# Kernel optimization log

Measured on AMD Instinct MI355X. Metric: run time of the kernel, lower is better.

The kernel has to match this reference:

```python
import jax, jax.numpy as jnp
import numpy as np

N_P, N_D, N_S = 100000, 1000, 5000      # patients, drugs, diseases
C, H, L = 64, 4, 2                       # hidden, heads, layers
DH = C // H                              # head dim
IN_P, IN_D, IN_S = 64, 128, 64           # raw feature dims per node type
E_PD, E_DP, E_DS, E_PS = 300000, 300000, 100000, 100000
EPS = 1e-16


def setup_inputs() -> dict:
    key = jax.random.key(0)
    ks = jax.random.split(key, 20)

    def lin(k, fin, fout, prefix=()):
        return jax.random.normal(k, prefix + (fin, fout), jnp.float32) / np.sqrt(fin).astype(np.float32)

    def edges(k, e, n_src, n_dst):
        k1, k2 = jax.random.split(k)
        return jnp.stack([jax.random.randint(k1, (e,), 0, n_src),
                          jax.random.randint(k2, (e,), 0, n_dst)]).astype(jnp.int32)

    inp = {}
    inp['x_p'] = jax.random.normal(ks[0], (N_P, IN_P), jnp.float32)
    inp['x_d'] = jax.random.normal(ks[1], (N_D, IN_D), jnp.float32)
    inp['x_s'] = jax.random.normal(ks[2], (N_S, IN_S), jnp.float32)
    inp['Win_p'] = lin(ks[3], IN_P, C); inp['bin_p'] = jnp.zeros((C,), jnp.float32)
    inp['Win_d'] = lin(ks[4], IN_D, C); inp['bin_d'] = jnp.zeros((C,), jnp.float32)
    inp['Win_s'] = lin(ks[5], IN_S, C); inp['bin_s'] = jnp.zeros((C,), jnp.float32)
    inp['Wk'] = lin(ks[6], C, C, (L, 3)); inp['bk'] = jnp.zeros((L, 3, C), jnp.float32)
    inp['Wq'] = lin(ks[7], C, C, (L, 3)); inp['bq'] = jnp.zeros((L, 3, C), jnp.float32)
    inp['Wv'] = lin(ks[8], C, C, (L, 3)); inp['bv'] = jnp.zeros((L, 3, C), jnp.float32)
    inp['Wa'] = lin(ks[9], C, C, (L, 3)); inp['ba'] = jnp.zeros((L, 3, C), jnp.float32)
    inp['a_rel'] = jax.random.normal(ks[10], (L, 4, H, DH, DH), jnp.float32) / np.sqrt(DH).astype(np.float32)
    inp['m_rel'] = jax.random.normal(ks[11], (L, 4, H, DH, DH), jnp.float32) / np.sqrt(DH).astype(np.float32)
    inp['p_rel'] = jnp.ones((L, 4, H), jnp.float32)   # PyG inits rel prior to ones
    inp['skip'] = jnp.ones((L, 3), jnp.float32)       # PyG inits skip gate to ones
    inp['ei_pd'] = edges(ks[12], E_PD, N_P, N_D)  # patient -takes-> drug
    inp['ei_dp'] = edges(ks[13], E_DP, N_D, N_P)  # drug -taken_by-> patient
    inp['ei_ds'] = edges(ks[14], E_DS, N_D, N_S)  # drug -treats-> disease
    inp['ei_ps'] = edges(ks[15], E_PS, N_P, N_S)  # patient -has-> disease
    return inp


def _hgt(x_p, x_d, x_s, Win_p, bin_p, Win_d, bin_d, Win_s, bin_s,
         Wk, bk, Wq, bq, Wv, bv, Wa, ba, a_rel, m_rel, p_rel, skip,
         ei_pd, ei_dp, ei_ds, ei_ps):
    Ns = (N_P, N_D, N_S)
    # per-node-type input projection (lin_dict)
    xs = [x_p @ Win_p + bin_p, x_d @ Win_d + bin_d, x_s @ Win_s + bin_s]
    # (src_type, dst_type, edge_index) for each relation
    edge_defs = [(0, 1, ei_pd), (1, 0, ei_dp), (1, 2, ei_ds), (0, 2, ei_ps)]
    inv_sqrt_d = np.float32(1.0 / np.sqrt(DH))

    for l in range(L):  # HGTConv layers
        k_t = [(xs[t] @ Wk[l, t] + bk[l, t]).reshape(Ns[t], H, DH) for t in range(3)]
        q_t = [(xs[t] @ Wq[l, t] + bq[l, t]).reshape(Ns[t], H, DH) for t in range(3)]
        v_t = [(xs[t] @ Wv[l, t] + bv[l, t]).reshape(Ns[t], H, DH) for t in range(3)]
        out = [jnp.zeros((Ns[t], H, DH), xs[t].dtype) for t in range(3)]
        for r, (st, dt, ei) in enumerate(edge_defs):
            src, dst = ei[0], ei[1]
            # relation-specific head-wise transforms of K and V
            k_rel = jnp.einsum('nhd,hde->nhe', k_t[st], a_rel[l, r])
            v_rel = jnp.einsum('nhd,hde->nhe', v_t[st], m_rel[l, r])
            # attention logits per edge, per head: [E, H]
            alpha = (q_t[dt][dst] * k_rel[src]).sum(-1) * (p_rel[l, r] * inv_sqrt_d)
            # segment softmax over incoming edges of each dst node (per relation)
            mx = jax.ops.segment_max(alpha, dst, num_segments=Ns[dt])
            a = jnp.exp(alpha - jax.lax.stop_gradient(mx)[dst])
            den = jax.ops.segment_sum(a, dst, num_segments=Ns[dt])
            a = a / (den[dst] + EPS)
            # attention-weighted scatter-add of messages, grouped by 'sum'
            out[dt] = out[dt] + jax.ops.segment_sum(v_rel[src] * a[:, :, None], dst, num_segments=Ns[dt])
        new_xs = []
        for t in range(3):
            o = jax.nn.gelu(out[t].reshape(Ns[t], C), approximate=False) @ Wa[l, t] + ba[l, t]
            s = jax.nn.sigmoid(skip[l, t])  # learned skip gate (in == out channels)
            new_xs.append(s * o + (1.0 - s) * xs[t])
        xs = new_xs
    # concatenate node-type outputs along node axis: [N_P+N_D+N_S, C]
    return jnp.concatenate(xs, axis=0)


def reference(x_p, x_d, x_s, Win_p, bin_p, Win_d, bin_d, Win_s, bin_s,
              Wk, bk, Wq, bq, Wv, bv, Wa, ba, a_rel, m_rel, p_rel, skip,
              ei_pd, ei_dp, ei_ds, ei_ps):
    return _hgt(x_p, x_d, x_s, Win_p, bin_p, Win_d, bin_d, Win_s, bin_s,
                Wk, bk, Wq, bq, Wv, bv, Wa, ba, a_rel, m_rel, p_rel, skip,
                ei_pd, ei_dp, ei_ds, ei_ps)
```

## Files before the change

kernel.cpp:

```cpp
#include <hip/hip_runtime.h>
#include <cmath>

typedef unsigned short ush;
typedef __attribute__((ext_vector_type(8))) short short8;
typedef __attribute__((ext_vector_type(4))) float floatx4;

static constexpr int N_P = 100000, N_D = 1000, N_S = 5000, NT = N_P + N_D + N_S;
static constexpr int NC = 111000;
static constexpr int E_TOT = 800000;

static constexpr int NB0 = 128, NB2 = 64, NB3 = 64;
static constexpr int CH0 = (300000 + NB0 - 1) / NB0;
static constexpr int CH2 = (100000 + NB2 - 1) / NB2;
static constexpr int HB0_OFF = 0;
static constexpr int HB2_OFF = NB0 * 1000;
static constexpr int HB3_OFF = HB2_OFF + NB2 * 5000;
static constexpr int NCH0 = NB0 / 16, NCH2 = NB2 / 16;
static constexpr int CS0_OFF = 0;
static constexpr int CS2_OFF = NCH0 * 1000;
static constexpr int CS3_OFF = CS2_OFF + NCH2 * 5000;
static constexpr int NHIST = NB0 + NB2 + NB3;
static constexpr int NBLK_R1 = (300000 + 255) / 256;
static constexpr int NZB = (100000 + 255) / 256;

__device__ __forceinline__ float b2f(ush b) { return __uint_as_float(((unsigned)b) << 16); }
__device__ __forceinline__ ush f2b(float f) {
    unsigned u = __float_as_uint(f);
    return (ush)((u + 0x7FFFu + ((u >> 16) & 1u)) >> 16);
}

static constexpr size_t OFF_WINP = 0;
static constexpr size_t OFF_BINP = 4096;
static constexpr size_t OFF_WIND = 4160;
static constexpr size_t OFF_BIND = 12352;
static constexpr size_t OFF_WINS = 12416;
static constexpr size_t OFF_BINS = 16512;
static constexpr size_t OFF_WK = 16576;
static constexpr size_t OFF_BK = 41152;
static constexpr size_t OFF_WQ = 41536;
static constexpr size_t OFF_BQ = 66112;
static constexpr size_t OFF_WV = 66496;
static constexpr size_t OFF_BV = 91072;
static constexpr size_t OFF_WA = 91456;
static constexpr size_t OFF_BA = 116032;
static constexpr size_t OFF_AREL = 116416;
static constexpr size_t OFF_MREL = 124608;
static constexpr size_t OFF_PREL = 132800;
static constexpr size_t OFF_SKIP = 132832;
static constexpr size_t CW_TOTAL = 132838;
static constexpr int NCONVB = (int)((CW_TOTAL + 255) / 256);
static constexpr int NSCB = (NC + 1 + 255) / 256;

struct ConvArgs {
    const void* src[18];
    long cum[19];
    int fl[18];
};

struct CsrB {
    const int* ei[3];
    const int* ei1;
};

__device__ __forceinline__ void hist_geom(int b, const CsrB& c, int& r, const int*& ei, int& E,
                                          int& ndst, int& e0, int& e1, int& hb) {
    if (b < NB0) {
        r = 0; ei = c.ei[0]; E = 300000; ndst = 1000;
        e0 = b * CH0; hb = HB0_OFF + b * 1000;
    } else if (b < NB0 + NB2) {
        r = 1; ei = c.ei[1]; E = 100000; ndst = 5000;
        e0 = (b - NB0) * CH2; hb = HB2_OFF + (b - NB0) * 5000;
    } else {
        r = 2; ei = c.ei[2]; E = 100000; ndst = 5000;
        e0 = (b - NB0 - NB2) * CH2; hb = HB3_OFF + (b - NB0 - NB2) * 5000;
    }
    e1 = min(E, e0 + ((r == 0) ? CH0 : CH2));
}

__device__ __forceinline__ bool cs_geom(int g, int& idx0, int& step) {
    if (g >= 48000) return false;
    if (g < 8000) {
        int c = g / 1000, d = g % 1000;
        idx0 = HB0_OFF + c * 16 * 1000 + d; step = 1000;
    } else if (g < 28000) {
        int gg = g - 8000, c = gg / 5000, d = gg % 5000;
        idx0 = HB2_OFF + c * 16 * 5000 + d; step = 5000;
    } else {
        int gg = g - 28000, c = gg / 5000, d = gg % 5000;
        idx0 = HB3_OFF + c * 16 * 5000 + d; step = 5000;
    }
    return true;
}

__global__ __launch_bounds__(256) void k1_kernel(ConvArgs a, ush* __restrict__ dst,
                                                 int* __restrict__ cnt_r1, CsrB c,
                                                 int* __restrict__ HB) {
    const int b = blockIdx.x;
    if (b < NCONVB) {
        long g = (long)b * 256 + threadIdx.x;
        if (g >= (long)CW_TOTAL) return;
        int t = 0;
        while (g >= a.cum[t + 1]) t++;
        long i = g - a.cum[t];
        float v = a.fl[t] ? ((const float*)a.src[t])[i] : b2f(((const ush*)a.src[t])[i]);
        dst[g] = f2b(v);
    } else if (b < NCONVB + NZB) {
        int g = (b - NCONVB) * 256 + threadIdx.x;
        if (g < 100000) cnt_r1[g] = 0;
    } else {
        __shared__ int h[5000];
        int r, E, ndst, e0, e1, hb;
        const int* ei;
        hist_geom(b - NCONVB - NZB, c, r, ei, E, ndst, e0, e1, hb);
        for (int d = threadIdx.x; d < ndst; d += 256) h[d] = 0;
        __syncthreads();
        for (int e = e0 + threadIdx.x; e < e1; e += 256) atomicAdd(&h[ei[E + e]], 1);
        __syncthreads();
        for (int d = threadIdx.x; d < ndst; d += 256) HB[hb + d] = h[d];
    }
}

template <int K>
__device__ __forceinline__ void stage_A(short* sA, const ush* __restrict__ X, int M, int row0) {
    for (int cid = threadIdx.x; cid < 64 * K / 8; cid += 256) {
        int r = cid / (K / 8), c0 = (cid % (K / 8)) * 8;
        int row = row0 + r;
        short8 v = {0, 0, 0, 0, 0, 0, 0, 0};
        if (row < M) v = *(const short8*)(const void*)(X + (size_t)row * K + c0);
        *(short8*)(&sA[r * (K + 8) + c0]) = v;
    }
}

template <int K>
__device__ __forceinline__ void stage_A_raw(short* sA, const void* __restrict__ X, int f,
                                            int M, int row0) {
    for (int cid = threadIdx.x; cid < 64 * K / 8; cid += 256) {
        int r = cid / (K / 8), c0 = (cid % (K / 8)) * 8;
        int row = row0 + r;
        short8 v = {0, 0, 0, 0, 0, 0, 0, 0};
        if (row < M) {
            if (f) {
                const floatx4* fp = (const floatx4*)((const float*)X + (size_t)row * K + c0);
                floatx4 f0 = fp[0], f1 = fp[1];
#pragma unroll
                for (int j = 0; j < 4; j++) v[j] = (short)f2b(f0[j]);
#pragma unroll
                for (int j = 0; j < 4; j++) v[4 + j] = (short)f2b(f1[j]);
            } else {
                v = *(const short8*)(const void*)((const ush*)X + (size_t)row * K + c0);
            }
        }
        *(short8*)(&sA[r * (K + 8) + c0]) = v;
    }
}

template <int K, int NOUT>
__device__ __forceinline__ void gemm_core(const short* sA, short* sB,
                                          const ush* __restrict__ W, const ush* __restrict__ Bb,
                                          ush* __restrict__ Y, int M, int row0) {
    constexpr int NF = (K / 32) * (NOUT / 16);
    const int tid = threadIdx.x;
    for (int u = tid; u < NF * 64; u += 256) {
        int f = u >> 6, l = u & 63;
        int s = f / (NOUT / 16), c = f % (NOUT / 16);
        int kbase = 32 * s + ((l >> 4) << 3), n = 16 * c + (l & 15);
        short8 v;
#pragma unroll
        for (int j = 0; j < 8; j++) v[j] = (short)W[(size_t)(kbase + j) * NOUT + n];
        *(short8*)(&sB[f * 512 + l * 8]) = v;
    }
    __syncthreads();
    const int w = tid >> 6, l = tid & 63;
    floatx4 acc[NOUT / 16];
#pragma unroll
    for (int c = 0; c < NOUT / 16; c++) {
        float bv = b2f(Bb[16 * c + (l & 15)]);
        acc[c] = (floatx4){bv, bv, bv, bv};
    }
#pragma unroll
    for (int s = 0; s < K / 32; s++) {
        short8 a = *(const short8*)(&sA[(16 * w + (l & 15)) * (K + 8) + 32 * s + ((l >> 4) << 3)]);
#pragma unroll
        for (int c = 0; c < NOUT / 16; c++) {
            short8 b = *(const short8*)(&sB[(s * (NOUT / 16) + c) * 512 + l * 8]);
            acc[c] = __builtin_amdgcn_mfma_f32_16x16x32_bf16(a, b, acc[c], 0, 0, 0);
        }
    }
#pragma unroll
    for (int c = 0; c < NOUT / 16; c++)
#pragma unroll
        for (int r = 0; r < 4; r++) {
            int row = row0 + 16 * w + ((l >> 4) << 2) + r;
            if (row < M) Y[(size_t)row * NOUT + 16 * c + (l & 15)] = f2b(acc[c][r]);
        }
}

template <int NG>
__device__ __forceinline__ void gemm_wide(const short* sA, short* sB,
                                          const ush* __restrict__ Wq, const ush* __restrict__ Bq,
                                          ush* __restrict__ Yq,
                                          const ush* __restrict__ WeA, ush* __restrict__ YA,
                                          const ush* __restrict__ WeB, ush* __restrict__ YB,
                                          int M, int row0) {
    constexpr int NF = 2 * NG;
    const int tid = threadIdx.x;
    for (int u = tid; u < NF * 64; u += 256) {
        int f = u >> 6, l = u & 63;
        int s = f / NG, c = f % NG;
        int kbase = 32 * s + ((l >> 4) << 3);
        const ush* W; int ld, cw;
        if (c < 4) { W = Wq; ld = 64; cw = 16 * c; }
        else if (c < 12) { W = WeA; ld = 128; cw = 16 * (c - 4); }
        else { W = WeB; ld = 128; cw = 16 * (c - 12); }
        int n = cw + (l & 15);
        short8 v;
#pragma unroll
        for (int j = 0; j < 8; j++) v[j] = (short)W[(size_t)(kbase + j) * ld + n];
        *(short8*)(&sB[f * 512 + l * 8]) = v;
    }
    __syncthreads();
    const int w = tid >> 6, l = tid & 63;
    floatx4 acc[NG];
#pragma unroll
    for (int c = 0; c < NG; c++) {
        float bv;
        if (c < 4) bv = b2f(Bq[16 * c + (l & 15)]);
        else if (c < 12) bv = b2f(WeA[8192 + 16 * (c - 4) + (l & 15)]);
        else bv = b2f(WeB[8192 + 16 * (c - 12) + (l & 15)]);
        acc[c] = (floatx4){bv, bv, bv, bv};
    }
#pragma unroll
    for (int s = 0; s < 2; s++) {
        short8 a = *(const short8*)(&sA[(16 * w + (l & 15)) * 72 + 32 * s + ((l >> 4) << 3)]);
#pragma unroll
        for (int c = 0; c < NG; c++) {
            short8 b = *(const short8*)(&sB[(s * NG + c) * 512 + l * 8]);
            acc[c] = __builtin_amdgcn_mfma_f32_16x16x32_bf16(a, b, acc[c], 0, 0, 0);
        }
    }
#pragma unroll
    for (int c = 0; c < NG; c++)
#pragma unroll
        for (int r = 0; r < 4; r++) {
            int row = row0 + 16 * w + ((l >> 4) << 2) + r;
            if (row >= M) continue;
            ush val = f2b(acc[c][r]);
            if (c < 4) Yq[(size_t)row * 64 + 16 * c + (l & 15)] = val;
            else if (c < 12) YA[(size_t)row * 128 + 16 * (c - 4) + (l & 15)] = val;
            else YB[(size_t)row * 128 + 16 * (c - 12) + (l & 15)] = val;
        }
}

struct K2Args {
    const void* raw[3];
    int f[3];
    const ush* W[3];
    const ush* Bb[3];
    ush* X;
    const int* HB;
    int* CS;
    int* cnt;
    const int* ei1;
};

__global__ __launch_bounds__(256) void k2_kernel(K2Args a) {
    extern __shared__ short smem[];
    const int b = blockIdx.x;
    if (b < 1658) {
        if (b < 1563) {
            short* sA = smem; short* sB = smem + 64 * 72;
            stage_A_raw<64>(sA, a.raw[0], a.f[0], N_P, b * 64);
            gemm_core<64, 64>(sA, sB, a.W[0], a.Bb[0], a.X, N_P, b * 64);
        } else if (b < 1579) {
            short* sA = smem; short* sB = smem + 64 * 136;
            stage_A_raw<128>(sA, a.raw[1], a.f[1], N_D, (b - 1563) * 64);
            gemm_core<128, 64>(sA, sB, a.W[1], a.Bb[1], a.X + (size_t)N_P * 64, N_D,
                               (b - 1563) * 64);
        } else {
            short* sA = smem; short* sB = smem + 64 * 72;
            stage_A_raw<64>(sA, a.raw[2], a.f[2], N_S, (b - 1579) * 64);
            gemm_core<64, 64>(sA, sB, a.W[2], a.Bb[2], a.X + (size_t)(N_P + N_D) * 64, N_S,
                              (b - 1579) * 64);
        }
    } else if (b < 1701) {
        int d = (b - 1658) * 256 + threadIdx.x;
        if (d >= 11000) return;
        int ld_, nch, base, step, cs0, csstep, roff;
        if (d < 1000) { ld_ = d; nch = NCH0; base = HB0_OFF + ld_; step = 1000;
                        cs0 = CS0_OFF + ld_; csstep = 1000; roff = 0; }
        else if (d < 6000) { ld_ = d - 1000; nch = NCH2; base = HB2_OFF + ld_; step = 5000;
                             cs0 = CS2_OFF + ld_; csstep = 5000; roff = 101000; }
        else { ld_ = d - 6000; nch = NCH2; base = HB3_OFF + ld_; step = 5000;
               cs0 = CS3_OFF + ld_; csstep = 5000; roff = 106000; }
        int run = 0;
        for (int cc = 0; cc < nch; cc++) {
            int s = 0;
#pragma unroll
            for (int bb = 0; bb < 16; bb++) s += a.HB[base + (cc * 16 + bb) * step];
            a.CS[cs0 + cc * csstep] = run;
            run += s;
        }
        a.cnt[roff + ld_] = run;
    } else {
        int g = (b - 1701) * 256 + threadIdx.x;
        if (g < 300000) atomicAdd(&a.cnt[1000 + a.ei1[300000 + g]], 1);
    }
}

__global__ __launch_bounds__(256) void k3_kernel(const int* __restrict__ cnt,
                                                 int* __restrict__ tmp,
                                                 int* __restrict__ part,
                                                 const ush* __restrict__ CW,
                                                 ush* __restrict__ weff) {
    const int b = blockIdx.x;
    if (b < 109) {
        __shared__ int ls[256];
        const int t = threadIdx.x;
        const int base = b * 1024 + t * 4;
        int v[4];
#pragma unroll
        for (int j = 0; j < 4; j++) v[j] = (base + j < NC) ? cnt[base + j] : 0;
        int tsum = v[0] + v[1] + v[2] + v[3];
        ls[t] = tsum;
        __syncthreads();
        for (int off = 1; off < 256; off <<= 1) {
            int y = (t >= off) ? ls[t - off] : 0;
            __syncthreads();
            ls[t] += y;
            __syncthreads();
        }
        int run = ls[t] - tsum;
#pragma unroll
        for (int j = 0; j < 4; j++) {
            if (base + j < NC) tmp[base + j] = run;
            run += v[j];
        }
        if (t == 255) part[b] = ls[255];
    } else {
        const int eb = b - 109;
        const int l = eb >> 2, r = eb & 3;
        const int st_of[4] = {0, 1, 1, 0};
        const int st = st_of[r];
        ush* out = weff + (size_t)eb * 8320;
        for (int idx = threadIdx.x; idx < 8320; idx += 256) {
            int n, k;
            if (idx < 8192) { k = idx >> 7; n = idx & 127; }
            else { k = -1; n = idx - 8192; }
            int kv = n >= 64;
            int j = n & 63, h = j >> 4, e = j & 15;
            const ush* W = CW + (kv ? OFF_WV : OFF_WK) + (size_t)(l * 3 + st) * 4096;
            const ush* B = CW + (kv ? OFF_BV : OFF_BK) + (size_t)(l * 3 + st) * 64;
            const ush* R = CW + (kv ? OFF_MREL : OFF_AREL) + (size_t)(l * 4 + r) * 1024;
            float acc = 0.f;
            if (k >= 0) {
#pragma unroll
                for (int d = 0; d < 16; d++)
                    acc += b2f(W[k * 64 + h * 16 + d]) * b2f(R[h * 256 + d * 16 + e]);
            } else {
#pragma unroll
                for (int d = 0; d < 16; d++)
                    acc += b2f(B[h * 16 + d]) * b2f(R[h * 256 + d * 16 + e]);
            }
            out[idx] = f2b(acc);
        }
    }
}

__global__ __launch_bounds__(256) void k4_kernel(const int* __restrict__ tmp,
                                                 const int* __restrict__ part,
                                                 int* __restrict__ rowptr,
                                                 int* __restrict__ HB,
                                                 const int* __restrict__ CS,
                                                 int* __restrict__ fillpos) {
    const int b = blockIdx.x;
    if (b < NSCB) {
        __shared__ int ls[256];
        const int t = threadIdx.x;
        ls[t] = (t < 109) ? part[t] : 0;
        __syncthreads();
        for (int off = 1; off < 256; off <<= 1) {
            int y = (t >= off) ? ls[t - off] : 0;
            __syncthreads();
            ls[t] += y;
            __syncthreads();
        }
        int i = b * 256 + t;
        if (i <= NC)
            rowptr[i] = (i == NC) ? ls[255] : tmp[i] + ((i >> 10) ? ls[(i >> 10) - 1] : 0);
    } else if (b < NSCB + 188) {
        int g = (b - NSCB) * 256 + threadIdx.x;
        int idx0, step;
        if (!cs_geom(g, idx0, step)) return;
        int run = CS[g];
#pragma unroll
        for (int bb = 0; bb < 16; bb++) {
            int t2 = HB[idx0 + bb * step];
            HB[idx0 + bb * step] = run;
            run += t2;
        }
    } else {
        int g = (b - NSCB - 188) * 256 + threadIdx.x;
        if (g < 100000) fillpos[g] = 0;
    }
}

struct QKVArgs {
    const ush* X;
    ush* Q;
    ush* KV[4];
    const ush* Wq[3];
    const ush* Bq[3];
    const ush* We[4];
    CsrB cb;
    const int* HB;
    const int* rowptr;
    int* fillpos;
    int* col;
};

__global__ __launch_bounds__(256) void qkvfill_kernel(QKVArgs a) {
    extern __shared__ short smem[];
    const int b = blockIdx.x;
    if (b < 1658) {
        short* sA = smem;
        short* sB = smem + 64 * 72;
        if (b < 1563) {
            stage_A<64>(sA, a.X, N_P, b * 64);
            gemm_wide<20>(sA, sB, a.Wq[0], a.Bq[0], a.Q, a.We[0], a.KV[0], a.We[3], a.KV[3],
                          N_P, b * 64);
        } else if (b < 1579) {
            int lb = b - 1563;
            stage_A<64>(sA, a.X + (size_t)N_P * 64, N_D, lb * 64);
            gemm_wide<20>(sA, sB, a.Wq[1], a.Bq[1], a.Q + (size_t)N_P * 64, a.We[1], a.KV[1],
                          a.We[2], a.KV[2], N_D, lb * 64);
        } else {
            int lb = b - 1579;
            stage_A<64>(sA, a.X + (size_t)(N_P + N_D) * 64, N_S, lb * 64);
            gemm_wide<4>(sA, sB, a.Wq[2], a.Bq[2], a.Q + (size_t)(N_P + N_D) * 64,
                         nullptr, nullptr, nullptr, nullptr, N_S, lb * 64);
        }
    } else if (b < 1658 + NHIST) {
        int* h = (int*)smem;
        int r, E, ndst, e0, e1, hb;
        const int* ei;
        hist_geom(b - 1658, a.cb, r, ei, E, ndst, e0, e1, hb);
        const int roff = (r == 0) ? 0 : (r == 1) ? 101000 : 106000;
        for (int d = threadIdx.x; d < ndst; d += 256) h[d] = a.rowptr[roff + d] + a.HB[hb + d];
        __syncthreads();
        for (int e = e0 + threadIdx.x; e < e1; e += 256) {
            int d = ei[E + e];
            int slot = atomicAdd(&h[d], 1);
            a.col[slot] = ei[e];
        }
    } else {
        int g = (b - 1658 - NHIST) * 256 + threadIdx.x;
        if (g < 300000) {
            int gi = 1000 + a.cb.ei1[300000 + g];
            int slot = a.rowptr[gi] + atomicAdd(&a.fillpos[gi], 1);
            a.col[slot] = a.cb.ei1[g];
        }
    }
}

struct AggrArgs {
    const int* rowptr;
    const int* col;
    const ush* KV[4];
    const ush* Q;
    const ush* prel;
    ush* OUT;
};

template <int LANES>
__device__ __forceinline__ void seg_attn(const AggrArgs& a, int rel, int g, int h, int lane,
                                         const float* qf, float* o) {
    const int s0 = a.rowptr[g], s1 = a.rowptr[g + 1];
    const ush* KV = a.KV[rel];
    const float ps = b2f(a.prel[rel * 4 + h]) * 0.25f;
    float m = -1e30f, s = 0.f;
    float acc[16];
#pragma unroll
    for (int i = 0; i < 16; i++) acc[i] = 0.f;
    for (int j = s0 + lane; j < s1; j += LANES) {
        int src = a.col[j];
        const ush* kp = KV + (size_t)src * 128 + h * 16;
        short8 k0 = *(const short8*)(const void*)kp;
        short8 k1 = *(const short8*)(const void*)(kp + 8);
        short8 v0 = *(const short8*)(const void*)(kp + 64);
        short8 v1 = *(const short8*)(const void*)(kp + 72);
        float dot = 0.f;
#pragma unroll
        for (int i = 0; i < 8; i++) dot += qf[i] * b2f((ush)k0[i]);
#pragma unroll
        for (int i = 0; i < 8; i++) dot += qf[8 + i] * b2f((ush)k1[i]);
        float aa = dot * ps;
        float nm = fmaxf(m, aa);
        float e0 = __expf(m - nm), e1 = __expf(aa - nm);
        s = s * e0 + e1;
#pragma unroll
        for (int i = 0; i < 8; i++) acc[i] = acc[i] * e0 + e1 * b2f((ush)v0[i]);
#pragma unroll
        for (int i = 0; i < 8; i++) acc[8 + i] = acc[8 + i] * e0 + e1 * b2f((ush)v1[i]);
        m = nm;
    }
#pragma unroll
    for (int wd = LANES >> 1; wd >= 1; wd >>= 1) {
        float mo = __shfl_xor(m, wd);
        float so = __shfl_xor(s, wd);
        float nm = fmaxf(m, mo);
        float e0 = __expf(m - nm), e1 = __expf(mo - nm);
        s = s * e0 + so * e1;
#pragma unroll
        for (int i = 0; i < 16; i++) {
            float ao = __shfl_xor(acc[i], wd);
            acc[i] = acc[i] * e0 + ao * e1;
        }
        m = nm;
    }
    float inv = 1.f / (s + 1e-16f);
#pragma unroll
    for (int i = 0; i < 16; i++) o[i] += acc[i] * inv;
}

template <int LANES>
__device__ __forceinline__ void job_run(const AggrArgs& a, int wid, int nd, int rel, int roff,
                                        size_t xoff, int rel2, int roff2) {
    const int lane = wid % LANES;
    const int grp = wid / LANES;
    const int d = grp >> 2, h = grp & 3;
    if (d >= nd) return;
    const ush* qp = a.Q + xoff + (size_t)d * 64 + h * 16;
    short8 q0 = *(const short8*)(const void*)qp;
    short8 q1 = *(const short8*)(const void*)(qp + 8);
    float qf[16];
#pragma unroll
    for (int i = 0; i < 8; i++) { qf[i] = b2f((ush)q0[i]); qf[8 + i] = b2f((ush)q1[i]); }
    float o[16];
#pragma unroll
    for (int i = 0; i < 16; i++) o[i] = 0.f;
    seg_attn<LANES>(a, rel, roff + d, h, lane, qf, o);
    if (rel2 >= 0) seg_attn<LANES>(a, rel2, roff2 + d, h, lane, qf, o);
    if (lane == 0) {
        ush* op = a.OUT + xoff + (size_t)d * 64 + h * 16;
        short8 w0, w1;
#pragma unroll
        for (int i = 0; i < 8; i++) {
            float va = o[i];
            w0[i] = (short)f2b(0.5f * va * (1.0f + erff(va * 0.70710678118654752f)));
            float vb = o[8 + i];
            w1[i] = (short)f2b(0.5f * vb * (1.0f + erff(vb * 0.70710678118654752f)));
        }
        *(short8*)(op) = w0;
        *(short8*)(op + 8) = w1;
    }
}

__global__ __launch_bounds__(256) void aggr_kernel(AggrArgs a) {
    const int b = blockIdx.x, t = threadIdx.x;
    if (b < 250) {
        job_run<16>(a, b * 256 + t, N_D, 0, 0, (size_t)N_P * 64, -1, 0);
    } else if (b < 563) {
        job_run<4>(a, (b - 250) * 256 + t, N_S, 2, 101000, (size_t)(N_P + N_D) * 64, 3, 106000);
    } else {
        job_run<2>(a, (b - 563) * 256 + t, N_P, 1, 1000, 0, -1, 0);
    }
}

struct EpiArgs {
    const ush* O;
    ush* X;
    const ush* W[3];
    const ush* Bb[3];
    const ush* skipv;
    void* fout;
    int foutf;
    int last;
};

__global__ __launch_bounds__(256) void epi_kernel(EpiArgs a) {
    const int b = blockIdx.x;
    int t, lb, M;
    size_t noff;
    if (b < 1563) { t = 0; lb = b; M = N_P; noff = 0; }
    else if (b < 1579) { t = 1; lb = b - 1563; M = N_D; noff = (size_t)N_P; }
    else { t = 2; lb = b - 1579; M = N_S; noff = (size_t)(N_P + N_D); }
    const ush* O = a.O + noff * 64;
    ush* X = a.X + noff * 64;
    const ush* W = a.W[t];
    __shared__ short sA[64 * 72];
    __shared__ short sB[8 * 512];
    const int tid = threadIdx.x;
    const int row0 = lb * 64;
    for (int cid = tid; cid < 512; cid += 256) {
        int r = cid >> 3, c0 = (cid & 7) * 8;
        int row = row0 + r;
        short8 sv = {0, 0, 0, 0, 0, 0, 0, 0};
        if (row < M) sv = *(const short8*)(const void*)(O + (size_t)row * 64 + c0);
        *(short8*)(&sA[r * 72 + c0]) = sv;
    }
    __syncthreads();
    const float sg = 1.f / (1.f + expf(-b2f(a.skipv[t])));
    for (int u = tid; u < 512; u += 256) {
        int f = u >> 6, l = u & 63;
        int s = f >> 2, c = f & 3;
        int kbase = 32 * s + ((l >> 4) << 3), n = 16 * c + (l & 15);
        short8 v;
#pragma unroll
        for (int j = 0; j < 8; j++) v[j] = (short)W[(size_t)(kbase + j) * 64 + n];
        *(short8*)(&sB[f * 512 + l * 8]) = v;
    }
    __syncthreads();
    const int w = tid >> 6, l = tid & 63;
    floatx4 acc[4];
#pragma unroll
    for (int c = 0; c < 4; c++) {
        float bv = b2f(a.Bb[t][16 * c + (l & 15)]);
        acc[c] = (floatx4){bv, bv, bv, bv};
    }
#pragma unroll
    for (int s = 0; s < 2; s++) {
        short8 av = *(const short8*)(&sA[(16 * w + (l & 15)) * 72 + 32 * s + ((l >> 4) << 3)]);
#pragma unroll
        for (int c = 0; c < 4; c++) {
            short8 bv = *(const short8*)(&sB[(s * 4 + c) * 512 + l * 8]);
            acc[c] = __builtin_amdgcn_mfma_f32_16x16x32_bf16(av, bv, acc[c], 0, 0, 0);
        }
    }
#pragma unroll
    for (int c = 0; c < 4; c++)
#pragma unroll
        for (int r = 0; r < 4; r++) {
            int row = row0 + 16 * w + ((l >> 4) << 2) + r;
            if (row >= M) continue;
            size_t off = (size_t)row * 64 + 16 * c + (l & 15);
            float val = sg * acc[c][r] + (1.f - sg) * b2f(X[off]);
            if (!a.last) {
                X[off] = f2b(val);
            } else {
                size_t goff = (noff + row) * 64 + 16 * c + (l & 15);
                if (a.foutf)
                    ((float*)a.fout)[goff] = val;
                else
                    ((ush*)a.fout)[goff] = f2b(val);
            }
        }
}

extern "C" void kernel_launch(void* const* d_in, const int* in_sizes, int n_in,
                              void* d_out, int out_size, void* d_ws, size_t ws_size,
                              hipStream_t stream) {
    char* w = (char*)d_ws;
    w += 64;
    ush* CW = (ush*)w;      w += ((CW_TOTAL * 2 + 63) / 64) * 64;
    ush* WEFFB = (ush*)w;   w += ((size_t)8 * 8320 * 2 + 63) / 64 * 64;
    ush* X = (ush*)w;       w += (size_t)NT * 64 * 2;
    ush* Q = (ush*)w;       w += (size_t)NT * 64 * 2;
    ush* KV0 = (ush*)w;     w += (size_t)N_P * 128 * 2;
    ush* KV1 = (ush*)w;     w += (size_t)N_D * 128 * 2;
    ush* KV2 = (ush*)w;     w += (size_t)N_D * 128 * 2;
    ush* KV3 = (ush*)w;     w += (size_t)N_P * 128 * 2;
    ush* OUT = (ush*)w;     w += (size_t)NT * 64 * 4;
    int* CNT = (int*)w;     w += (size_t)NC * 4;
    int* TMP = (int*)w;     w += (size_t)NC * 4;
    int* PART = (int*)w;    w += 512;
    int* ROWPTR = (int*)w;  w += (size_t)(NC + 1) * 4;
    int* COL = (int*)w;     w += (size_t)E_TOT * 4;
    int* HB = (int*)OUT;
    int* CS = (int*)OUT + 800000;

    static const long sz[18] = {4096, 64, 8192, 64, 4096, 64, 24576, 384, 24576, 384,
                                24576, 384, 24576, 384, 8192, 8192, 32, 6};
    ConvArgs ca;
    long cum = 0;
    for (int t = 0; t < 18; t++) {
        ca.src[t] = d_in[3 + t];
        ca.cum[t] = cum;
        ca.fl[t] = (in_sizes[3 + t] != (int)(sz[t] * 2)) ? 1 : 0;
        cum += sz[t];
    }
    ca.cum[18] = cum;

    CsrB cb;
    cb.ei[0] = (const int*)d_in[21];
    cb.ei[1] = (const int*)d_in[23];
    cb.ei[2] = (const int*)d_in[24];
    cb.ei1 = (const int*)d_in[22];

    k1_kernel<<<NCONVB + NZB + NHIST, 256, 0, stream>>>(ca, CW, CNT + 1000, cb, HB);

    K2Args k2;
    k2.raw[0] = d_in[0]; k2.f[0] = (in_sizes[0] != N_P * 64 * 2) ? 1 : 0;
    k2.raw[1] = d_in[1]; k2.f[1] = (in_sizes[1] != N_D * 128 * 2) ? 1 : 0;
    k2.raw[2] = d_in[2]; k2.f[2] = (in_sizes[2] != N_S * 64 * 2) ? 1 : 0;
    k2.W[0] = CW + OFF_WINP; k2.Bb[0] = CW + OFF_BINP;
    k2.W[1] = CW + OFF_WIND; k2.Bb[1] = CW + OFF_BIND;
    k2.W[2] = CW + OFF_WINS; k2.Bb[2] = CW + OFF_BINS;
    k2.X = X;
    k2.HB = HB; k2.CS = CS; k2.cnt = CNT; k2.ei1 = cb.ei1;
    k2_kernel<<<1701 + NBLK_R1, 256, 33792, stream>>>(k2);

    k3_kernel<<<109 + 8, 256, 0, stream>>>(CNT, TMP, PART, CW, WEFFB);

    k4_kernel<<<NSCB + 188 + NZB, 256, 0, stream>>>(TMP, PART, ROWPTR, HB, CS, CNT + 1000);

    ush* KVr[4] = {KV0, KV1, KV2, KV3};
    const int foutf = (out_size != NT * 64 * 2) ? 1 : 0;

    for (int l = 0; l < 2; l++) {
        QKVArgs qk;
        qk.X = X;
        qk.Q = Q;
        for (int r = 0; r < 4; r++) {
            qk.KV[r] = KVr[r];
            qk.We[r] = WEFFB + (size_t)(l * 4 + r) * 8320;
        }
        for (int t = 0; t < 3; t++) {
            qk.Wq[t] = CW + OFF_WQ + (size_t)(l * 3 + t) * 4096;
            qk.Bq[t] = CW + OFF_BQ + (l * 3 + t) * 64;
        }
        qk.cb = cb;
        qk.HB = HB;
        qk.rowptr = ROWPTR;
        qk.fillpos = CNT;
        qk.col = COL;
        const int qgrid = (l == 0) ? (1658 + NHIST + NBLK_R1) : 1658;
        qkvfill_kernel<<<qgrid, 256, 50176, stream>>>(qk);

        AggrArgs aa;
        aa.rowptr = ROWPTR;
        aa.col = COL;
        for (int r = 0; r < 4; r++) aa.KV[r] = KVr[r];
        aa.Q = Q;
        aa.prel = CW + OFF_PREL + l * 16;
        aa.OUT = OUT;
        aggr_kernel<<<3688, 256, 0, stream>>>(aa);

        EpiArgs ea;
        ea.O = OUT;
        ea.X = X;
        for (int t = 0; t < 3; t++) {
            ea.W[t] = CW + OFF_WA + (size_t)(l * 3 + t) * 4096;
            ea.Bb[t] = CW + OFF_BA + (l * 3 + t) * 64;
        }
        ea.skipv = CW + OFF_SKIP + l * 3;
        ea.fout = d_out;
        ea.foutf = foutf;
        ea.last = (l == 1) ? 1 : 0;
        epi_kernel<<<1658, 256, 0, stream>>>(ea);
    }
}
```

Baseline: 369.3 us.

## Pre-swizzle weights into MFMA fragment layout and stage outputs through LDS

Weights for the input projection, Q and output projections are pre-permuted once, in k1, into the MFMA B-fragment order. The GEMM kernels then read B fragments straight from global memory instead of building per-block LDS copies with strided scalar loads. K and V are split into separate 64-wide arrays, and GEMM outputs are staged through LDS so each thread writes 16-byte rows, coalesced. This lowers LDS usage and lifts occupancy, but adds extra barriers and relies on L1/L2 hits for the repeated global weight reads.

```diff
diff --git a/kernel.cpp b/kernel.cpp
--- a/kernel.cpp
+++ b/kernel.cpp
@@ -51,6 +51,14 @@
 static constexpr int NCONVB = (int)((CW_TOTAL + 255) / 256);
 static constexpr int NSCB = (NC + 1 + 255) / 256;
 
+static constexpr size_t TWINP = 0;
+static constexpr size_t TWIND = 4096;
+static constexpr size_t TWINS = 12288;
+static constexpr size_t TWQO = 16384;
+static constexpr size_t TWAO = 40960;
+static constexpr size_t TW_TOTAL = 65536;
+static constexpr int NTWB = (int)(TW_TOTAL / 256);
+
 struct ConvArgs {
     const void* src[18];
     long cum[19];
@@ -93,6 +101,7 @@
 }
 
 __global__ __launch_bounds__(256) void k1_kernel(ConvArgs a, ush* __restrict__ dst,
+                                                 ush* __restrict__ tw,
                                                  int* __restrict__ cnt_r1, CsrB c,
                                                  int* __restrict__ HB) {
     const int b = blockIdx.x;
@@ -107,7 +116,7 @@
     } else if (b < NCONVB + NZB) {
         int g = (b - NCONVB) * 256 + threadIdx.x;
         if (g < 100000) cnt_r1[g] = 0;
-    } else {
+    } else if (b < NCONVB + NZB + NHIST) {
         __shared__ int h[5000];
         int r, E, ndst, e0, e1, hb;
         const int* ei;
@@ -117,6 +126,21 @@
         for (int e = e0 + threadIdx.x; e < e1; e += 256) atomicAdd(&h[ei[E + e]], 1);
         __syncthreads();
         for (int d = threadIdx.x; d < ndst; d += 256) HB[hb + d] = h[d];
+    } else {
+        int g = (b - NCONVB - NZB - NHIST) * 256 + threadIdx.x;
+        const void* src; int fl; long ibase; int e;
+        if (g < 4096) { src = a.src[0]; fl = a.fl[0]; e = g; ibase = 0; }
+        else if (g < 12288) { src = a.src[2]; fl = a.fl[2]; e = g - 4096; ibase = 0; }
+        else if (g < 16384) { src = a.src[4]; fl = a.fl[4]; e = g - 12288; ibase = 0; }
+        else if (g < 40960) { int ee = g - 16384; src = a.src[8]; fl = a.fl[8];
+                              e = ee & 4095; ibase = (long)(ee >> 12) * 4096; }
+        else { int ee = g - 40960; src = a.src[12]; fl = a.fl[12];
+               e = ee & 4095; ibase = (long)(ee >> 12) * 4096; }
+        int f = e >> 9, l = (e >> 3) & 63, j = e & 7;
+        int s = f >> 2, cc = f & 3;
+        long in = ibase + (long)(32 * s + ((l >> 4) << 3) + j) * 64 + 16 * cc + (l & 15);
+        float v = fl ? ((const float*)src)[in] : b2f(((const ush*)src)[in]);
+        tw[g] = f2b(v);
     }
 }
 
@@ -154,26 +178,16 @@
     }
 }
 
-template <int K, int NOUT>
-__device__ __forceinline__ void gemm_core(const short* sA, short* sB,
-                                          const ush* __restrict__ W, const ush* __restrict__ Bb,
-                                          ush* __restrict__ Y, int M, int row0) {
-    constexpr int NF = (K / 32) * (NOUT / 16);
+template <int K>
+__device__ __forceinline__ void gemm_direct64(short* sA, const ush* __restrict__ WF,
+                                              const ush* __restrict__ Bb,
+                                              ush* __restrict__ Y, int M, int row0) {
+    __syncthreads();
     const int tid = threadIdx.x;
-    for (int u = tid; u < NF * 64; u += 256) {
-        int f = u >> 6, l = u & 63;
-        int s = f / (NOUT / 16), c = f % (NOUT / 16);
-        int kbase = 32 * s + ((l >> 4) << 3), n = 16 * c + (l & 15);
-        short8 v;
-#pragma unroll
-        for (int j = 0; j < 8; j++) v[j] = (short)W[(size_t)(kbase + j) * NOUT + n];
-        *(short8*)(&sB[f * 512 + l * 8]) = v;
-    }
-    __syncthreads();
     const int w = tid >> 6, l = tid & 63;
-    floatx4 acc[NOUT / 16];
-#pragma unroll
-    for (int c = 0; c < NOUT / 16; c++) {
+    floatx4 acc[4];
+#pragma unroll
+    for (int c = 0; c < 4; c++) {
         float bv = b2f(Bb[16 * c + (l & 15)]);
         acc[c] = (floatx4){bv, bv, bv, bv};
     }
@@ -181,44 +195,37 @@
     for (int s = 0; s < K / 32; s++) {
         short8 a = *(const short8*)(&sA[(16 * w + (l & 15)) * (K + 8) + 32 * s + ((l >> 4) << 3)]);
 #pragma unroll
-        for (int c = 0; c < NOUT / 16; c++) {
-            short8 b = *(const short8*)(&sB[(s * (NOUT / 16) + c) * 512 + l * 8]);
+        for (int c = 0; c < 4; c++) {
+            short8 b = *(const short8*)(const void*)(WF + ((size_t)(s * 4 + c) * 64 + l) * 8);
             acc[c] = __builtin_amdgcn_mfma_f32_16x16x32_bf16(a, b, acc[c], 0, 0, 0);
         }
     }
-#pragma unroll
-    for (int c = 0; c < NOUT / 16; c++)
-#pragma unroll
-        for (int r = 0; r < 4; r++) {
-            int row = row0 + 16 * w + ((l >> 4) << 2) + r;
-            if (row < M) Y[(size_t)row * NOUT + 16 * c + (l & 15)] = f2b(acc[c][r]);
-        }
+    __syncthreads();
+#pragma unroll
+    for (int c = 0; c < 4; c++)
+#pragma unroll
+        for (int r = 0; r < 4; r++)
+            sA[(16 * w + ((l >> 4) << 2) + r) * 72 + 16 * c + (l & 15)] = (short)f2b(acc[c][r]);
+    __syncthreads();
+    for (int u = tid; u < 512; u += 256) {
+        int r = u >> 3, c0 = (u & 7) * 8;
+        int row = row0 + r;
+        if (row < M)
+            *(short8*)(Y + (size_t)row * 64 + c0) = *(const short8*)(&sA[r * 72 + c0]);
+    }
 }
 
 template <int NG>
-__device__ __forceinline__ void gemm_wide(const short* sA, short* sB,
-                                          const ush* __restrict__ Wq, const ush* __restrict__ Bq,
-                                          ush* __restrict__ Yq,
-                                          const ush* __restrict__ WeA, ush* __restrict__ YA,
-                                          const ush* __restrict__ WeB, ush* __restrict__ YB,
-                                          int M, int row0) {
-    constexpr int NF = 2 * NG;
+__device__ __forceinline__ void gemm_wideD(short* sA,
+                                           const ush* __restrict__ Wq,
+                                           const ush* __restrict__ Bq, ush* __restrict__ Yq,
+                                           const ush* __restrict__ WeA,
+                                           ush* __restrict__ YAk, ush* __restrict__ YAv,
+                                           const ush* __restrict__ WeB,
+                                           ush* __restrict__ YBk, ush* __restrict__ YBv,
+                                           int M, int row0) {
+    __syncthreads();
     const int tid = threadIdx.x;
-    for (int u = tid; u < NF * 64; u += 256) {
-        int f = u >> 6, l = u & 63;
-        int s = f / NG, c = f % NG;
-        int kbase = 32 * s + ((l >> 4) << 3);
-        const ush* W; int ld, cw;
-        if (c < 4) { W = Wq; ld = 64; cw = 16 * c; }
-        else if (c < 12) { W = WeA; ld = 128; cw = 16 * (c - 4); }
-        else { W = WeB; ld = 128; cw = 16 * (c - 12); }
-        int n = cw + (l & 15);
-        short8 v;
-#pragma unroll
-        for (int j = 0; j < 8; j++) v[j] = (short)W[(size_t)(kbase + j) * ld + n];
-        *(short8*)(&sB[f * 512 + l * 8]) = v;
-    }
-    __syncthreads();
     const int w = tid >> 6, l = tid & 63;
     floatx4 acc[NG];
 #pragma unroll
@@ -234,21 +241,33 @@
         short8 a = *(const short8*)(&sA[(16 * w + (l & 15)) * 72 + 32 * s + ((l >> 4) << 3)]);
 #pragma unroll
         for (int c = 0; c < NG; c++) {
-            short8 b = *(const short8*)(&sB[(s * NG + c) * 512 + l * 8]);
+            const ush* bp;
+            if (c < 4) bp = Wq + ((size_t)(s * 4 + c) * 64 + l) * 8;
+            else if (c < 12) bp = WeA + ((size_t)(s * 8 + (c - 4)) * 64 + l) * 8;
+            else bp = WeB + ((size_t)(s * 8 + (c - 12)) * 64 + l) * 8;
+            short8 b = *(const short8*)(const void*)bp;
             acc[c] = __builtin_amdgcn_mfma_f32_16x16x32_bf16(a, b, acc[c], 0, 0, 0);
         }
     }
-#pragma unroll
-    for (int c = 0; c < NG; c++)
-#pragma unroll
-        for (int r = 0; r < 4; r++) {
-            int row = row0 + 16 * w + ((l >> 4) << 2) + r;
-            if (row >= M) continue;
-            ush val = f2b(acc[c][r]);
-            if (c < 4) Yq[(size_t)row * 64 + 16 * c + (l & 15)] = val;
-            else if (c < 12) YA[(size_t)row * 128 + 16 * (c - 4) + (l & 15)] = val;
-            else YB[(size_t)row * 128 + 16 * (c - 12) + (l & 15)] = val;
-        }
+    ush* dst[5] = {Yq, YAk, YAv, YBk, YBv};
+#pragma unroll
+    for (int cg = 0; cg < NG / 4; cg++) {
+        __syncthreads();
+#pragma unroll
+        for (int c2 = 0; c2 < 4; c2++)
+#pragma unroll
+            for (int r = 0; r < 4; r++)
+                sA[(16 * w + ((l >> 4) << 2) + r) * 72 + 16 * c2 + (l & 15)] =
+                    (short)f2b(acc[cg * 4 + c2][r]);
+        __syncthreads();
+        ush* Y = dst[cg];
+        for (int u = tid; u < 512; u += 256) {
+            int r = u >> 3, c0 = (u & 7) * 8;
+            int row = row0 + r;
+            if (row < M)
+                *(short8*)(Y + (size_t)row * 64 + c0) = *(const short8*)(&sA[r * 72 + c0]);
+        }
+    }
 }
 
 struct K2Args {
@@ -267,19 +286,17 @@
     extern __shared__ short smem[];
     const int b = blockIdx.x;
     if (b < 1658) {
+        short* sA = smem;
         if (b < 1563) {
-            short* sA = smem; short* sB = smem + 64 * 72;
             stage_A_raw<64>(sA, a.raw[0], a.f[0], N_P, b * 64);
-            gemm_core<64, 64>(sA, sB, a.W[0], a.Bb[0], a.X, N_P, b * 64);
+            gemm_direct64<64>(sA, a.W[0], a.Bb[0], a.X, N_P, b * 64);
         } else if (b < 1579) {
-            short* sA = smem; short* sB = smem + 64 * 136;
             stage_A_raw<128>(sA, a.raw[1], a.f[1], N_D, (b - 1563) * 64);
-            gemm_core<128, 64>(sA, sB, a.W[1], a.Bb[1], a.X + (size_t)N_P * 64, N_D,
+            gemm_direct64<128>(sA, a.W[1], a.Bb[1], a.X + (size_t)N_P * 64, N_D,
                                (b - 1563) * 64);
         } else {
-            short* sA = smem; short* sB = smem + 64 * 72;
             stage_A_raw<64>(sA, a.raw[2], a.f[2], N_S, (b - 1579) * 64);
-            gemm_core<64, 64>(sA, sB, a.W[2], a.Bb[2], a.X + (size_t)(N_P + N_D) * 64, N_S,
+            gemm_direct64<64>(sA, a.W[2], a.Bb[2], a.X + (size_t)(N_P + N_D) * 64, N_S,
                               (b - 1579) * 64);
         }
     } else if (b < 1701) {
@@ -343,11 +360,15 @@
         const int st = st_of[r];
         ush* out = weff + (size_t)eb * 8320;
         for (int idx = threadIdx.x; idx < 8320; idx += 256) {
-            int n, k;
-            if (idx < 8192) { k = idx >> 7; n = idx & 127; }
-            else { k = -1; n = idx - 8192; }
+            int k, n;
+            if (idx < 8192) {
+                int f = idx >> 9, ll = (idx >> 3) & 63, j = idx & 7;
+                int s = f >> 3, c = f & 7;
+                k = 32 * s + ((ll >> 4) << 3) + j;
+                n = 16 * c + (ll & 15);
+            } else { k = -1; n = idx - 8192; }
             int kv = n >= 64;
-            int j = n & 63, h = j >> 4, e = j & 15;
+            int jj = n & 63, h = jj >> 4, e = jj & 15;
             const ush* W = CW + (kv ? OFF_WV : OFF_WK) + (size_t)(l * 3 + st) * 4096;
             const ush* B = CW + (kv ? OFF_BV : OFF_BK) + (size_t)(l * 3 + st) * 64;
             const ush* R = CW + (kv ? OFF_MREL : OFF_AREL) + (size_t)(l * 4 + r) * 1024;
@@ -407,7 +428,8 @@
 struct QKVArgs {
     const ush* X;
     ush* Q;
-    ush* KV[4];
+    ush* KVk[4];
+    ush* KVv[4];
     const ush* Wq[3];
     const ush* Bq[3];
     const ush* We[4];
@@ -423,21 +445,23 @@
     const int b = blockIdx.x;
     if (b < 1658) {
         short* sA = smem;
-        short* sB = smem + 64 * 72;
         if (b < 1563) {
             stage_A<64>(sA, a.X, N_P, b * 64);
-            gemm_wide<20>(sA, sB, a.Wq[0], a.Bq[0], a.Q, a.We[0], a.KV[0], a.We[3], a.KV[3],
-                          N_P, b * 64);
+            gemm_wideD<20>(sA, a.Wq[0], a.Bq[0], a.Q,
+                           a.We[0], a.KVk[0], a.KVv[0],
+                           a.We[3], a.KVk[3], a.KVv[3], N_P, b * 64);
         } else if (b < 1579) {
             int lb = b - 1563;
             stage_A<64>(sA, a.X + (size_t)N_P * 64, N_D, lb * 64);
-            gemm_wide<20>(sA, sB, a.Wq[1], a.Bq[1], a.Q + (size_t)N_P * 64, a.We[1], a.KV[1],
-                          a.We[2], a.KV[2], N_D, lb * 64);
+            gemm_wideD<20>(sA, a.Wq[1], a.Bq[1], a.Q + (size_t)N_P * 64,
+                           a.We[1], a.KVk[1], a.KVv[1],
+                           a.We[2], a.KVk[2], a.KVv[2], N_D, lb * 64);
         } else {
             int lb = b - 1579;
             stage_A<64>(sA, a.X + (size_t)(N_P + N_D) * 64, N_S, lb * 64);
-            gemm_wide<4>(sA, sB, a.Wq[2], a.Bq[2], a.Q + (size_t)(N_P + N_D) * 64,
-                         nullptr, nullptr, nullptr, nullptr, N_S, lb * 64);
+            gemm_wideD<4>(sA, a.Wq[2], a.Bq[2], a.Q + (size_t)(N_P + N_D) * 64,
+                          nullptr, nullptr, nullptr, nullptr, nullptr, nullptr,
+                          N_S, lb * 64);
         }
     } else if (b < 1658 + NHIST) {
         int* h = (int*)smem;
@@ -465,7 +489,8 @@
 struct AggrArgs {
     const int* rowptr;
     const int* col;
-    const ush* KV[4];
+    const ush* KVk[4];
+    const ush* KVv[4];
     const ush* Q;
     const ush* prel;
     ush* OUT;
@@ -475,7 +500,8 @@
 __device__ __forceinline__ void seg_attn(const AggrArgs& a, int rel, int g, int h, int lane,
                                          const float* qf, float* o) {
     const int s0 = a.rowptr[g], s1 = a.rowptr[g + 1];
-    const ush* KV = a.KV[rel];
+    const ush* Kb = a.KVk[rel];
+    const ush* Vb = a.KVv[rel];
     const float ps = b2f(a.prel[rel * 4 + h]) * 0.25f;
     float m = -1e30f, s = 0.f;
     float acc[16];
@@ -483,11 +509,12 @@
     for (int i = 0; i < 16; i++) acc[i] = 0.f;
     for (int j = s0 + lane; j < s1; j += LANES) {
         int src = a.col[j];
-        const ush* kp = KV + (size_t)src * 128 + h * 16;
+        const ush* kp = Kb + (size_t)src * 64 + h * 16;
+        const ush* vp = Vb + (size_t)src * 64 + h * 16;
         short8 k0 = *(const short8*)(const void*)kp;
         short8 k1 = *(const short8*)(const void*)(kp + 8);
-        short8 v0 = *(const short8*)(const void*)(kp + 64);
-        short8 v1 = *(const short8*)(const void*)(kp + 72);
+        short8 v0 = *(const short8*)(const void*)vp;
+        short8 v1 = *(const short8*)(const void*)(vp + 8);
         float dot = 0.f;
 #pragma unroll
         for (int i = 0; i < 8; i++) dot += qf[i] * b2f((ush)k0[i]);
@@ -586,9 +613,8 @@
     else { t = 2; lb = b - 1579; M = N_S; noff = (size_t)(N_P + N_D); }
     const ush* O = a.O + noff * 64;
     ush* X = a.X + noff * 64;
-    const ush* W = a.W[t];
+    const ush* WF = a.W[t];
     __shared__ short sA[64 * 72];
-    __shared__ short sB[8 * 512];
     const int tid = threadIdx.x;
     const int row0 = lb * 64;
     for (int cid = tid; cid < 512; cid += 256) {
@@ -600,16 +626,6 @@
     }
     __syncthreads();
     const float sg = 1.f / (1.f + expf(-b2f(a.skipv[t])));
-    for (int u = tid; u < 512; u += 256) {
-        int f = u >> 6, l = u & 63;
-        int s = f >> 2, c = f & 3;
-        int kbase = 32 * s + ((l >> 4) << 3), n = 16 * c + (l & 15);
-        short8 v;
-#pragma unroll
-        for (int j = 0; j < 8; j++) v[j] = (short)W[(size_t)(kbase + j) * 64 + n];
-        *(short8*)(&sB[f * 512 + l * 8]) = v;
-    }
-    __syncthreads();
     const int w = tid >> 6, l = tid & 63;
     floatx4 acc[4];
 #pragma unroll
@@ -622,28 +638,59 @@
         short8 av = *(const short8*)(&sA[(16 * w + (l & 15)) * 72 + 32 * s + ((l >> 4) << 3)]);
 #pragma unroll
         for (int c = 0; c < 4; c++) {
-            short8 bv = *(const short8*)(&sB[(s * 4 + c) * 512 + l * 8]);
+            short8 bv = *(const short8*)(const void*)(WF + ((size_t)(s * 4 + c) * 64 + l) * 8);
             acc[c] = __builtin_amdgcn_mfma_f32_16x16x32_bf16(av, bv, acc[c], 0, 0, 0);
         }
     }
-#pragma unroll
-    for (int c = 0; c < 4; c++)
-#pragma unroll
-        for (int r = 0; r < 4; r++) {
-            int row = row0 + 16 * w + ((l >> 4) << 2) + r;
-            if (row >= M) continue;
-            size_t off = (size_t)row * 64 + 16 * c + (l & 15);
-            float val = sg * acc[c][r] + (1.f - sg) * b2f(X[off]);
-            if (!a.last) {
-                X[off] = f2b(val);
-            } else {
-                size_t goff = (noff + row) * 64 + 16 * c + (l & 15);
-                if (a.foutf)
-                    ((float*)a.fout)[goff] = val;
-                else
-                    ((ush*)a.fout)[goff] = f2b(val);
+    float* sOf = (float*)sA;
+#pragma unroll
+    for (int ch = 0; ch < 2; ch++) {
+        __syncthreads();
+        if ((w >> 1) == ch) {
+#pragma unroll
+            for (int c = 0; c < 4; c++)
+#pragma unroll
+                for (int r = 0; r < 4; r++)
+                    sOf[(16 * (w & 1) + ((l >> 4) << 2) + r) * 68 + 16 * c + (l & 15)] =
+                        acc[c][r];
+        }
+        __syncthreads();
+        {
+            int r = tid >> 3, c0 = (tid & 7) * 8;
+            int row = row0 + ch * 32 + r;
+            if (row < M) {
+                floatx4 f0 = *(const floatx4*)(&sOf[r * 68 + c0]);
+                floatx4 f1 = *(const floatx4*)(&sOf[r * 68 + c0 + 4]);
+                short8 xv = *(const short8*)(const void*)(X + (size_t)row * 64 + c0);
+                float vo[8];
+#pragma unroll
+                for (int j = 0; j < 4; j++) vo[j] = sg * f0[j] + (1.f - sg) * b2f((ush)xv[j]);
+#pragma unroll
+                for (int j = 0; j < 4; j++)
+                    vo[4 + j] = sg * f1[j] + (1.f - sg) * b2f((ush)xv[4 + j]);
+                if (!a.last) {
+                    short8 ov;
+#pragma unroll
+                    for (int j = 0; j < 8; j++) ov[j] = (short)f2b(vo[j]);
+                    *(short8*)(X + (size_t)row * 64 + c0) = ov;
+                } else {
+                    size_t goff = (noff + row) * 64 + c0;
+                    if (a.foutf) {
+                        floatx4 o0, o1;
+#pragma unroll
+                        for (int j = 0; j < 4; j++) { o0[j] = vo[j]; o1[j] = vo[4 + j]; }
+                        *(floatx4*)((float*)a.fout + goff) = o0;
+                        *(floatx4*)((float*)a.fout + goff + 4) = o1;
+                    } else {
+                        short8 ov;
+#pragma unroll
+                        for (int j = 0; j < 8; j++) ov[j] = (short)f2b(vo[j]);
+                        *(short8*)((ush*)a.fout + goff) = ov;
+                    }
+                }
             }
         }
+    }
 }
 
 extern "C" void kernel_launch(void* const* d_in, const int* in_sizes, int n_in,
@@ -653,6 +700,7 @@
     w += 64;
     ush* CW = (ush*)w;      w += ((CW_TOTAL * 2 + 63) / 64) * 64;
     ush* WEFFB = (ush*)w;   w += ((size_t)8 * 8320 * 2 + 63) / 64 * 64;
+    ush* TW = (ush*)w;      w += (size_t)TW_TOTAL * 2;
     ush* X = (ush*)w;       w += (size_t)NT * 64 * 2;
     ush* Q = (ush*)w;       w += (size_t)NT * 64 * 2;
     ush* KV0 = (ush*)w;     w += (size_t)N_P * 128 * 2;
@@ -686,24 +734,25 @@
     cb.ei[2] = (const int*)d_in[24];
     cb.ei1 = (const int*)d_in[22];
 
-    k1_kernel<<<NCONVB + NZB + NHIST, 256, 0, stream>>>(ca, CW, CNT + 1000, cb, HB);
+    k1_kernel<<<NCONVB + NZB + NHIST + NTWB, 256, 0, stream>>>(ca, CW, TW, CNT + 1000, cb, HB);
 
     K2Args k2;
     k2.raw[0] = d_in[0]; k2.f[0] = (in_sizes[0] != N_P * 64 * 2) ? 1 : 0;
     k2.raw[1] = d_in[1]; k2.f[1] = (in_sizes[1] != N_D * 128 * 2) ? 1 : 0;
     k2.raw[2] = d_in[2]; k2.f[2] = (in_sizes[2] != N_S * 64 * 2) ? 1 : 0;
-    k2.W[0] = CW + OFF_WINP; k2.Bb[0] = CW + OFF_BINP;
-    k2.W[1] = CW + OFF_WIND; k2.Bb[1] = CW + OFF_BIND;
-    k2.W[2] = CW + OFF_WINS; k2.Bb[2] = CW + OFF_BINS;
+    k2.W[0] = TW + TWINP; k2.Bb[0] = CW + OFF_BINP;
+    k2.W[1] = TW + TWIND; k2.Bb[1] = CW + OFF_BIND;
+    k2.W[2] = TW + TWINS; k2.Bb[2] = CW + OFF_BINS;
     k2.X = X;
     k2.HB = HB; k2.CS = CS; k2.cnt = CNT; k2.ei1 = cb.ei1;
-    k2_kernel<<<1701 + NBLK_R1, 256, 33792, stream>>>(k2);
+    k2_kernel<<<1701 + NBLK_R1, 256, 17408, stream>>>(k2);
 
     k3_kernel<<<109 + 8, 256, 0, stream>>>(CNT, TMP, PART, CW, WEFFB);
 
     k4_kernel<<<NSCB + 188 + NZB, 256, 0, stream>>>(TMP, PART, ROWPTR, HB, CS, CNT + 1000);
 
     ush* KVr[4] = {KV0, KV1, KV2, KV3};
+    const size_t nsr[4] = {(size_t)N_P, (size_t)N_D, (size_t)N_D, (size_t)N_P};
     const int foutf = (out_size != NT * 64 * 2) ? 1 : 0;
 
     for (int l = 0; l < 2; l++) {
@@ -711,11 +760,12 @@
         qk.X = X;
         qk.Q = Q;
         for (int r = 0; r < 4; r++) {
-            qk.KV[r] = KVr[r];
+            qk.KVk[r] = KVr[r];
+            qk.KVv[r] = KVr[r] + nsr[r] * 64;
             qk.We[r] = WEFFB + (size_t)(l * 4 + r) * 8320;
         }
         for (int t = 0; t < 3; t++) {
-            qk.Wq[t] = CW + OFF_WQ + (size_t)(l * 3 + t) * 4096;
+            qk.Wq[t] = TW + TWQO + (size_t)(l * 3 + t) * 4096;
             qk.Bq[t] = CW + OFF_BQ + (l * 3 + t) * 64;
         }
         qk.cb = cb;
@@ -724,12 +774,16 @@
         qk.fillpos = CNT;
         qk.col = COL;
         const int qgrid = (l == 0) ? (1658 + NHIST + NBLK_R1) : 1658;
-        qkvfill_kernel<<<qgrid, 256, 50176, stream>>>(qk);
+        const int qlds = (l == 0) ? 20000 : 9216;
+        qkvfill_kernel<<<qgrid, 256, qlds, stream>>>(qk);
 
         AggrArgs aa;
         aa.rowptr = ROWPTR;
         aa.col = COL;
-        for (int r = 0; r < 4; r++) aa.KV[r] = KVr[r];
+        for (int r = 0; r < 4; r++) {
+            aa.KVk[r] = KVr[r];
+            aa.KVv[r] = KVr[r] + nsr[r] * 64;
+        }
         aa.Q = Q;
         aa.prel = CW + OFF_PREL + l * 16;
         aa.OUT = OUT;
@@ -739,7 +793,7 @@
         ea.O = OUT;
         ea.X = X;
         for (int t = 0; t < 3; t++) {
-            ea.W[t] = CW + OFF_WA + (size_t)(l * 3 + t) * 4096;
+            ea.W[t] = TW + TWAO + (size_t)(l * 3 + t) * 4096;
             ea.Bb[t] = CW + OFF_BA + (l * 3 + t) * 64;
         }
         ea.skipv = CW + OFF_SKIP + l * 3;
```

New measurement: 401.8 us. 8.8% more time.
